# Kernel tuning notes

Hardware: AMD Instinct MI355X
Metric: run time of the kernel (lower is better)

The kernel has to match this reference:

```python
import jax, jax.numpy as jnp
import numpy as np

LN_EPS = 1e-5


def setup_inputs() -> dict:
    key = jax.random.key(0)
    k1, k2 = jax.random.split(key)
    N, S, D, H = 2048, 8, 512, 8
    VAR = 2 ** S - 1  # 255 lattice elements
    x = jax.random.normal(k1, (N, S, D), dtype=jnp.float32)
    # FM ~ 1/S + 0.1*noise, clipped like standardize() keeps it in [0, 1]
    FM = jnp.clip(1.0 / S + 0.1 * jax.random.normal(k2, (VAR, H), dtype=jnp.float32), 0.0, 1.0)
    ln_weight = jnp.ones((H, D), dtype=jnp.float32)
    ln_bias = jnp.zeros((H, D), dtype=jnp.float32)
    prelu_w = jnp.full((1,), 0.25, dtype=jnp.float32)  # torch PReLU default
    return {"x": x, "FM": FM, "ln_weight": ln_weight, "ln_bias": ln_bias, "prelu_w": prelu_w}


def reference(x, FM, ln_weight, ln_bias, prelu_w):
    # x: (N, S, D); FM: (2^S-1, H)
    N, S, D = x.shape
    # descending sort along source axis
    sortIdx = jnp.argsort(-x, axis=1)                       # (N, S, D) in [0, S)
    x_sort = jnp.take_along_axis(x, sortIdx, axis=1)        # (N, S, D)
    # successive differences with implicit trailing zero
    x_shift = jnp.concatenate([x_sort[:, 1:, :], jnp.zeros((N, 1, D), x.dtype)], axis=1)
    d = x_sort - x_shift                                    # (N, S, D)
    # lattice indices: cumsum of 2^idx, minus 1
    latt = jnp.cumsum(jnp.power(2, sortIdx).astype(jnp.int32), axis=1) - 1  # (N, S, D)
    FM_ = FM[latt]                                          # (N, S, D, H) gather
    y = jnp.einsum('bsn,bsnh->bhn', d, FM_)                 # (N, H, D)
    # LayerNorm over normalized_shape=(H, D)
    mean = jnp.mean(y, axis=(1, 2), keepdims=True)
    var = jnp.mean(jnp.square(y - mean), axis=(1, 2), keepdims=True)
    y = (y - mean) * jax.lax.rsqrt(var + LN_EPS) * ln_weight + ln_bias
    # PReLU (single shared parameter); dropout p=0.0 -> identity
    y = jnp.where(y > 0, y, prelu_w[0] * y)
    return y
```

## Files before the change

kernel.cpp:

```cpp
#include <hip/hip_runtime.h>

#define LN_EPS 1e-5f

__global__ __launch_bounds__(512) void choquet_fused_kernel(
    const float* __restrict__ x,
    const float* __restrict__ FM,
    const float* __restrict__ lnw,
    const float* __restrict__ lnb,
    const float* __restrict__ prelu,
    float* __restrict__ out)
{
    constexpr int S = 8, D = 512, H = 8;
    __shared__ float fm_s[255 * 9];
    __shared__ float red[16];
    __shared__ float stats[2];

    const int n = blockIdx.x;
    const int d = threadIdx.x;

    for (int i = threadIdx.x; i < 255 * 8; i += 512) {
        int r = i >> 3, c = i & 7;
        fm_s[r * 9 + c] = FM[i];
    }
    __syncthreads();

    const float* xp = x + (size_t)n * S * D + d;
    float v0 = xp[0 * D], v1 = xp[1 * D], v2 = xp[2 * D], v3 = xp[3 * D];
    float v4 = xp[4 * D], v5 = xp[5 * D], v6 = xp[6 * D], v7 = xp[7 * D];
    int i0 = 0, i1 = 1, i2 = 2, i3 = 3, i4 = 4, i5 = 5, i6 = 6, i7 = 7;

#define CE(a, b)                                                              \
    {                                                                         \
        bool sw = (v##a < v##b) || (v##a == v##b && i##a > i##b);             \
        if (sw) {                                                             \
            float tv = v##a; v##a = v##b; v##b = tv;                          \
            int   ti = i##a; i##a = i##b; i##b = ti;                          \
        }                                                                     \
    }
    CE(0, 1) CE(2, 3) CE(4, 5) CE(6, 7)
    CE(0, 2) CE(1, 3) CE(4, 6) CE(5, 7)
    CE(1, 2) CE(5, 6) CE(0, 4) CE(3, 7)
    CE(1, 5) CE(2, 6)
    CE(1, 4) CE(3, 6)
    CE(2, 4) CE(3, 5)
    CE(3, 4)
#undef CE

    float y[H];
#pragma unroll
    for (int h = 0; h < H; ++h) y[h] = 0.f;

    int mask = 0;
#define STEP(vs, is, vnext)                                                   \
    {                                                                         \
        mask |= (1 << (is));                                                  \
        const float diff = (vs) - (vnext);                                    \
        const float* row = &fm_s[(mask - 1) * 9];                             \
        _Pragma("unroll")                                                     \
        for (int h = 0; h < H; ++h) y[h] += diff * row[h];                    \
    }
    STEP(v0, i0, v1)
    STEP(v1, i1, v2)
    STEP(v2, i2, v3)
    STEP(v3, i3, v4)
    STEP(v4, i4, v5)
    STEP(v5, i5, v6)
    STEP(v6, i6, v7)
    STEP(v7, i7, 0.0f)
#undef STEP

    float s1 = 0.f, s2 = 0.f;
#pragma unroll
    for (int h = 0; h < H; ++h) { s1 += y[h]; s2 += y[h] * y[h]; }
#pragma unroll
    for (int off = 32; off > 0; off >>= 1) {
        s1 += __shfl_down(s1, off);
        s2 += __shfl_down(s2, off);
    }
    const int wid = threadIdx.x >> 6;
    const int lane = threadIdx.x & 63;
    if (lane == 0) { red[wid * 2] = s1; red[wid * 2 + 1] = s2; }
    __syncthreads();
    if (threadIdx.x == 0) {
        float t1 = 0.f, t2 = 0.f;
#pragma unroll
        for (int w = 0; w < 8; ++w) { t1 += red[w * 2]; t2 += red[w * 2 + 1]; }
        const float mean = t1 * (1.0f / 4096.0f);
        float var = t2 * (1.0f / 4096.0f) - mean * mean;
        var = var < 0.f ? 0.f : var;
        stats[0] = mean;
        stats[1] = rsqrtf(var + LN_EPS);
    }
    __syncthreads();

    const float mean = stats[0];
    const float rstd = stats[1];
    const float pw = prelu[0];
    float* op = out + (size_t)n * H * D + d;
#pragma unroll
    for (int h = 0; h < H; ++h) {
        float val = (y[h] - mean) * rstd * lnw[h * D + d] + lnb[h * D + d];
        op[h * D] = val > 0.f ? val : pw * val;
    }
}

extern "C" void kernel_launch(void* const* d_in, const int* in_sizes, int n_in,
                              void* d_out, int out_size, void* d_ws, size_t ws_size,
                              hipStream_t stream) {
    const float* x     = (const float*)d_in[0];
    const float* FM    = (const float*)d_in[1];
    const float* lnw   = (const float*)d_in[2];
    const float* lnb   = (const float*)d_in[3];
    const float* prelu = (const float*)d_in[4];
    float* out = (float*)d_out;

    const int N = 2048;
    choquet_fused_kernel<<<N, 512, 0, stream>>>(x, FM, lnw, lnb, prelu, out);
}
```

Baseline: 25.34 us.

## Overlap FM staging with sort, vectorize LDS rows, remove a block barrier

FM staging into shared memory now uses float4 global loads and float2 LDS rows padded to stride 5. The barrier is deferred until after the sorting network, so global loads of x, LN weights and FM overlap. LN weight/bias loads are hoisted to the start of the kernel. The final reduction lets every thread sum the per-wave partials itself, which removes one __syncthreads and the stats broadcast at the cost of a few redundant LDS reads per thread. N is also derived from the input size.

```diff
diff --git a/kernel.cpp b/kernel.cpp
--- a/kernel.cpp
+++ b/kernel.cpp
@@ -11,22 +11,28 @@
     float* __restrict__ out)
 {
     constexpr int S = 8, D = 512, H = 8;
-    __shared__ float fm_s[255 * 9];
+    __shared__ float2 fm_s[255 * 5];
     __shared__ float red[16];
-    __shared__ float stats[2];
 
     const int n = blockIdx.x;
     const int d = threadIdx.x;
 
-    for (int i = threadIdx.x; i < 255 * 8; i += 512) {
-        int r = i >> 3, c = i & 7;
-        fm_s[r * 9 + c] = FM[i];
-    }
-    __syncthreads();
-
     const float* xp = x + (size_t)n * S * D + d;
     float v0 = xp[0 * D], v1 = xp[1 * D], v2 = xp[2 * D], v3 = xp[3 * D];
     float v4 = xp[4 * D], v5 = xp[5 * D], v6 = xp[6 * D], v7 = xp[7 * D];
+
+    float w[H], b[H];
+#pragma unroll
+    for (int h = 0; h < H; ++h) { w[h] = lnw[h * D + d]; b[h] = lnb[h * D + d]; }
+    const float pw = prelu[0];
+
+    if (threadIdx.x < 510) {
+        const float4 v = ((const float4*)FM)[threadIdx.x];
+        const int r = threadIdx.x >> 1, half = threadIdx.x & 1;
+        fm_s[5 * r + 2 * half]     = make_float2(v.x, v.y);
+        fm_s[5 * r + 2 * half + 1] = make_float2(v.z, v.w);
+    }
+
     int i0 = 0, i1 = 1, i2 = 2, i3 = 3, i4 = 4, i5 = 5, i6 = 6, i7 = 7;
 
 #define CE(a, b)                                                              \
@@ -46,6 +52,8 @@
     CE(3, 4)
 #undef CE
 
+    __syncthreads();
+
     float y[H];
 #pragma unroll
     for (int h = 0; h < H; ++h) y[h] = 0.f;
@@ -55,9 +63,12 @@
     {                                                                         \
         mask |= (1 << (is));                                                  \
         const float diff = (vs) - (vnext);                                    \
-        const float* row = &fm_s[(mask - 1) * 9];                             \
-        _Pragma("unroll")                                                     \
-        for (int h = 0; h < H; ++h) y[h] += diff * row[h];                    \
+        const float2* row = &fm_s[5 * (mask - 1)];                            \
+        const float2 r0 = row[0], r1 = row[1], r2 = row[2], r3 = row[3];      \
+        y[0] += diff * r0.x; y[1] += diff * r0.y;                             \
+        y[2] += diff * r1.x; y[3] += diff * r1.y;                             \
+        y[4] += diff * r2.x; y[5] += diff * r2.y;                             \
+        y[6] += diff * r3.x; y[7] += diff * r3.y;                             \
     }
     STEP(v0, i0, v1)
     STEP(v1, i1, v2)
@@ -74,32 +85,25 @@
     for (int h = 0; h < H; ++h) { s1 += y[h]; s2 += y[h] * y[h]; }
 #pragma unroll
     for (int off = 32; off > 0; off >>= 1) {
-        s1 += __shfl_down(s1, off);
-        s2 += __shfl_down(s2, off);
+        s1 += __shfl_xor(s1, off);
+        s2 += __shfl_xor(s2, off);
     }
     const int wid = threadIdx.x >> 6;
-    const int lane = threadIdx.x & 63;
-    if (lane == 0) { red[wid * 2] = s1; red[wid * 2 + 1] = s2; }
-    __syncthreads();
-    if (threadIdx.x == 0) {
-        float t1 = 0.f, t2 = 0.f;
-#pragma unroll
-        for (int w = 0; w < 8; ++w) { t1 += red[w * 2]; t2 += red[w * 2 + 1]; }
-        const float mean = t1 * (1.0f / 4096.0f);
-        float var = t2 * (1.0f / 4096.0f) - mean * mean;
-        var = var < 0.f ? 0.f : var;
-        stats[0] = mean;
-        stats[1] = rsqrtf(var + LN_EPS);
-    }
+    if ((threadIdx.x & 63) == 0) { red[wid * 2] = s1; red[wid * 2 + 1] = s2; }
     __syncthreads();
 
-    const float mean = stats[0];
-    const float rstd = stats[1];
-    const float pw = prelu[0];
+    float t1 = 0.f, t2 = 0.f;
+#pragma unroll
+    for (int wv = 0; wv < 8; ++wv) { t1 += red[wv * 2]; t2 += red[wv * 2 + 1]; }
+    const float mean = t1 * (1.0f / 4096.0f);
+    float var = t2 * (1.0f / 4096.0f) - mean * mean;
+    var = var < 0.f ? 0.f : var;
+    const float rstd = rsqrtf(var + LN_EPS);
+
     float* op = out + (size_t)n * H * D + d;
 #pragma unroll
     for (int h = 0; h < H; ++h) {
-        float val = (y[h] - mean) * rstd * lnw[h * D + d] + lnb[h * D + d];
+        float val = (y[h] - mean) * rstd * w[h] + b[h];
         op[h * D] = val > 0.f ? val : pw * val;
     }
 }
@@ -114,6 +118,6 @@
     const float* prelu = (const float*)d_in[4];
     float* out = (float*)d_out;
 
-    const int N = 2048;
+    const int N = in_sizes[0] / (8 * 512);
     choquet_fused_kernel<<<N, 512, 0, stream>>>(x, FM, lnw, lnb, prelu, out);
 }
```

Result: faster. 24.55 us (-3.1%).
